# Kernel optimization log

Measured on AMD Instinct MI355X. Metric: run time of the kernel, lower is better.

The kernel has to match this reference:

```python
import jax, jax.numpy as jnp
import numpy as np
import math

S, B, E, H = 2048, 2, 1024, 16
D = E // H
LN_EPS = 1e-5


def setup_inputs() -> dict:
    key = jax.random.key(0)
    ks = jax.random.split(key, 8)
    src = jax.random.normal(ks[0], (S, B, E), dtype=jnp.float32)
    # causal attention mask: 1 = attend, 0 = masked
    src_mask = jnp.tril(jnp.ones((S, S), dtype=jnp.int32))
    in_proj_w = jax.random.normal(ks[1], (2 * E, E), dtype=jnp.float32) * 0.02
    in_proj_b = jnp.zeros((2 * E,), dtype=jnp.float32)
    out_proj_w = jax.random.normal(ks[2], (E, E), dtype=jnp.float32) * 0.02
    out_proj_b = jnp.zeros((E,), dtype=jnp.float32)
    ln_g = jnp.ones((E,), dtype=jnp.float32)
    ln_b = jnp.zeros((E,), dtype=jnp.float32)
    return {"src": src, "src_mask": src_mask, "in_proj_w": in_proj_w,
            "in_proj_b": in_proj_b, "out_proj_w": out_proj_w,
            "out_proj_b": out_proj_b, "ln_g": ln_g, "ln_b": ln_b}


def _layernorm(x, g, b):
    mu = jnp.mean(x, axis=-1, keepdims=True)
    var = jnp.mean(jnp.square(x - mu), axis=-1, keepdims=True)
    return (x - mu) * jax.lax.rsqrt(var + LN_EPS) * g + b


def reference(src, src_mask, in_proj_w, in_proj_b, out_proj_w, out_proj_b, ln_g, ln_b):
    # src: (S, B, E)
    x_norm = _layernorm(src, ln_g, ln_b)
    proj = jax.nn.silu(x_norm @ in_proj_w.T + in_proj_b)     # (S, B, 2E)
    qkv, u = jnp.split(proj, 2, axis=-1)                     # each (S, B, E)
    qkv = qkv.reshape(S, B, H, D)                            # q = k = v = qkv
    # scores: (B, H, S_q, S_k)
    scores = jnp.einsum('sbhd,tbhd->bhst', qkv, qkv) / math.sqrt(D)
    # torch does masked_fill(-inf) then silu; silu(-inf) -> 0 in the limit,
    # which is the intended semantics (masked positions contribute nothing).
    weights = jnp.where(src_mask[None, None, :, :] == 0, 0.0, jax.nn.silu(scores))
    # attn_dropout is identity at eval
    attn = jnp.einsum('bhst,tbhd->sbhd', weights, qkv).reshape(S, B, E)
    gated = attn * u
    out = src + (gated @ out_proj_w.T + out_proj_b)          # out_dropout = identity
    return out
```

## Files before the change

kernel.cpp:

```cpp
#include <hip/hip_runtime.h>


typedef __attribute__((ext_vector_type(8))) short  short8;
typedef __attribute__((ext_vector_type(4))) float  floatx4;
typedef __attribute__((ext_vector_type(4))) float  fvec4;
typedef __attribute__((ext_vector_type(4))) unsigned short usvec4;
typedef __attribute__((ext_vector_type(4))) int    intx4;

__device__ __forceinline__ unsigned short f2b(float f) {
  unsigned u = __builtin_bit_cast(unsigned, f);
  u += 0x7FFFu + ((u >> 16) & 1u);
  return (unsigned short)(u >> 16);
}
__device__ __forceinline__ float b2f(unsigned short h) {
  unsigned u = ((unsigned)h) << 16;
  return __builtin_bit_cast(float, u);
}
__device__ __forceinline__ float silu_f(float x) {
  float e = __builtin_amdgcn_exp2f(-1.44269504f * x);
  return x * __builtin_amdgcn_rcpf(1.f + e);
}
__device__ __forceinline__ void async_copy16(void* lds, const void* g) {
  __builtin_amdgcn_global_load_lds(
      (__attribute__((address_space(1))) void*)(g),
      (__attribute__((address_space(3))) void*)(lds), 16, 0, 0);
}

__global__ __launch_bounds__(256) void prep_kernel(
    const float* __restrict__ w1, unsigned short* __restrict__ w1b,
    const float* __restrict__ w2, unsigned short* __restrict__ w2b,
    const float* __restrict__ x, const float* __restrict__ g,
    const float* __restrict__ b, unsigned short* __restrict__ xn) {
  const int blk = blockIdx.x;
  if (blk < 3072) {
    int i = blk * 256 + threadIdx.x;
    const float* s; unsigned short* d; int j;
    if (i < 524288) { s = w1; d = w1b; j = i; } else { s = w2; d = w2b; j = i - 524288; }
    fvec4 v = ((const fvec4*)s)[j];
    usvec4 o = { f2b(v.x), f2b(v.y), f2b(v.z), f2b(v.w) };
    ((usvec4*)d)[j] = o;
    return;
  }
  const int lane = threadIdx.x & 63;
  const int row = (blk - 3072) * 4 + (threadIdx.x >> 6);
  const fvec4* xr = (const fvec4*)(x + (long)row * 1024);
  fvec4 v[4];
  float s = 0.f, s2 = 0.f;
  #pragma unroll
  for (int c = 0; c < 4; ++c) {
    v[c] = xr[lane + 64 * c];
    s  += v[c].x + v[c].y + v[c].z + v[c].w;
    s2 += v[c].x*v[c].x + v[c].y*v[c].y + v[c].z*v[c].z + v[c].w*v[c].w;
  }
  #pragma unroll
  for (int off = 32; off; off >>= 1) { s += __shfl_xor(s, off); s2 += __shfl_xor(s2, off); }
  float mu  = s * (1.f / 1024.f);
  float var = s2 * (1.f / 1024.f) - mu * mu;
  float rs  = rsqrtf(var + 1e-5f);
  usvec4* outr = (usvec4*)(xn + (long)row * 1024);
  #pragma unroll
  for (int c = 0; c < 4; ++c) {
    fvec4 gg = ((const fvec4*)g)[lane + 64 * c];
    fvec4 bb = ((const fvec4*)b)[lane + 64 * c];
    usvec4 o = { f2b((v[c].x - mu) * rs * gg.x + bb.x),
                 f2b((v[c].y - mu) * rs * gg.y + bb.y),
                 f2b((v[c].z - mu) * rs * gg.z + bb.z),
                 f2b((v[c].w - mu) * rs * gg.w + bb.w) };
    outr[lane + 64 * c] = o;
  }
}

__global__ __launch_bounds__(256, 2) void gemm_in(
    const unsigned short* __restrict__ A, const unsigned short* __restrict__ Bw,
    const float* __restrict__ bias,
    unsigned short* __restrict__ out0, unsigned short* __restrict__ out1) {
  __shared__ __align__(16) unsigned short sA[2][128 * 32];
  __shared__ __align__(16) unsigned short sB[2][128 * 32];
  const int t = threadIdx.x;
  const int lane = t & 63, l15 = lane & 15, quad = lane >> 4;
  const int w = t >> 6, wm = w >> 1, wn = w & 1;
  const int m0 = blockIdx.y * 128, n0 = blockIdx.x * 128;
  const int K = 1024;

  floatx4 acc[4][4];
  const floatx4 z4 = {0.f, 0.f, 0.f, 0.f};
  #pragma unroll
  for (int i = 0; i < 4; i++)
    #pragma unroll
    for (int j = 0; j < 4; j++) acc[i][j] = z4;

  for (int kt = 0; kt < 16; ++kt) {
    const int k0 = kt << 6;
    __syncthreads();
    #pragma unroll
    for (int h = 0; h < 2; ++h) {
      #pragma unroll
      for (int c = 0; c < 2; ++c) {
        int slot = c * 256 + t;
        int row = slot >> 2, col = (slot & 3) << 3;
        async_copy16(&sA[h][slot * 8], &A[(m0 + row) * K + k0 + h * 32 + col]);
        async_copy16(&sB[h][slot * 8], &Bw[(n0 + row) * K + k0 + h * 32 + col]);
      }
    }
    __syncthreads();
    #pragma unroll
    for (int h = 0; h < 2; ++h) {
      short8 af[4], bf[4];
      #pragma unroll
      for (int mr = 0; mr < 4; mr++)
        af[mr] = *(const short8*)&sA[h][(wm * 64 + mr * 16 + l15) * 32 + quad * 8];
      #pragma unroll
      for (int nr = 0; nr < 4; nr++)
        bf[nr] = *(const short8*)&sB[h][(wn * 64 + nr * 16 + l15) * 32 + quad * 8];
      #pragma unroll
      for (int mr = 0; mr < 4; mr++)
        #pragma unroll
        for (int nr = 0; nr < 4; nr++)
          acc[mr][nr] = __builtin_amdgcn_mfma_f32_16x16x32_bf16(af[mr], bf[nr], acc[mr][nr], 0, 0, 0);
    }
  }

  #pragma unroll
  for (int mr = 0; mr < 4; mr++) {
    int gm0 = m0 + wm * 64 + mr * 16 + quad * 4;
    #pragma unroll
    for (int nr = 0; nr < 4; nr++) {
      int gn = n0 + wn * 64 + nr * 16 + l15;
      float bv = bias[gn];
      unsigned short* dst = (gn < 1024) ? (out0 + gn) : (out1 + gn - 1024);
      #pragma unroll
      for (int r = 0; r < 4; r++) {
        float v = acc[mr][nr][r] + bv;
        dst[(long)(gm0 + r) * 1024] = f2b(silu_f(v));
      }
    }
  }
}

__global__ __launch_bounds__(256, 2) void gemm_out(
    const unsigned short* __restrict__ A, const unsigned short* __restrict__ Bw,
    const float* __restrict__ bias, const float* __restrict__ src,
    float* __restrict__ outf) {
  __shared__ __align__(16) unsigned short sA[2][128 * 32];
  __shared__ __align__(16) unsigned short sB[2][64 * 32];
  const int t = threadIdx.x;
  const int lane = t & 63, l15 = lane & 15, quad = lane >> 4;
  const int w = t >> 6;
  const int m0 = blockIdx.y * 128, n0 = blockIdx.x * 64;

  floatx4 acc[2][4];
  const floatx4 z4 = {0.f, 0.f, 0.f, 0.f};
  #pragma unroll
  for (int i = 0; i < 2; i++)
    #pragma unroll
    for (int j = 0; j < 4; j++) acc[i][j] = z4;

  for (int kt = 0; kt < 16; ++kt) {
    const int k0 = kt << 6;
    __syncthreads();
    #pragma unroll
    for (int h = 0; h < 2; ++h) {
      #pragma unroll
      for (int c = 0; c < 2; ++c) {
        int slot = c * 256 + t;
        int row = slot >> 2, col = (slot & 3) << 3;
        async_copy16(&sA[h][slot * 8], &A[(m0 + row) * 1024 + k0 + h * 32 + col]);
      }
      { int row = t >> 2, col = (t & 3) << 3;
        async_copy16(&sB[h][t * 8], &Bw[(n0 + row) * 1024 + k0 + h * 32 + col]); }
    }
    __syncthreads();
    #pragma unroll
    for (int h = 0; h < 2; ++h) {
      short8 af[2], bf[4];
      #pragma unroll
      for (int mr = 0; mr < 2; mr++)
        af[mr] = *(const short8*)&sA[h][(w * 32 + mr * 16 + l15) * 32 + quad * 8];
      #pragma unroll
      for (int nr = 0; nr < 4; nr++)
        bf[nr] = *(const short8*)&sB[h][(nr * 16 + l15) * 32 + quad * 8];
      #pragma unroll
      for (int mr = 0; mr < 2; mr++)
        #pragma unroll
        for (int nr = 0; nr < 4; nr++)
          acc[mr][nr] = __builtin_amdgcn_mfma_f32_16x16x32_bf16(af[mr], bf[nr], acc[mr][nr], 0, 0, 0);
    }
  }

  #pragma unroll
  for (int mr = 0; mr < 2; mr++) {
    int gm0 = m0 + w * 32 + mr * 16 + quad * 4;
    #pragma unroll
    for (int nr = 0; nr < 4; nr++) {
      int gn = n0 + nr * 16 + l15;
      float bv = bias[gn];
      #pragma unroll
      for (int r = 0; r < 4; r++) {
        long idx = (long)(gm0 + r) * 1024 + gn;
        outf[idx] = acc[mr][nr][r] + bv + src[idx];
      }
    }
  }
}

#define SKS 72
#define SVS 136
__device__ __forceinline__ void write_kv(unsigned short* sKp, unsigned short* sVp,
                                         const short8* kv, int rg, int dg, int swz0) {
  #pragma unroll
  for (int i = 0; i < 4; ++i)
    *(short8*)&sKp[(rg * 4 + i) * SKS + dg * 8] = kv[i];
  intx4 k0 = __builtin_bit_cast(intx4, kv[0]);
  intx4 k1 = __builtin_bit_cast(intx4, kv[1]);
  intx4 k2 = __builtin_bit_cast(intx4, kv[2]);
  intx4 k3 = __builtin_bit_cast(intx4, kv[3]);
  #pragma unroll
  for (int jj = 0; jj < 4; ++jj) {
    unsigned lo = __builtin_amdgcn_perm((unsigned)k1[jj], (unsigned)k0[jj], 0x05040100u);
    unsigned hi = __builtin_amdgcn_perm((unsigned)k3[jj], (unsigned)k2[jj], 0x05040100u);
    int j = 2 * jj, d = dg * 8 + j;
    int gsw = (swz0 + j) & 15;
    *(unsigned long long*)&sVp[d * SVS + gsw * 8 + (rg & 1) * 4] =
        (unsigned long long)lo | ((unsigned long long)hi << 32);
    lo = __builtin_amdgcn_perm((unsigned)k1[jj], (unsigned)k0[jj], 0x07060302u);
    hi = __builtin_amdgcn_perm((unsigned)k3[jj], (unsigned)k2[jj], 0x07060302u);
    j = 2 * jj + 1; d = dg * 8 + j;
    gsw = (swz0 + j) & 15;
    *(unsigned long long*)&sVp[d * SVS + gsw * 8 + (rg & 1) * 4] =
        (unsigned long long)lo | ((unsigned long long)hi << 32);
  }
}

__global__ __launch_bounds__(256, 2) void attn_kernel(
    const unsigned short* __restrict__ qkv, const unsigned short* __restrict__ u,
    unsigned short* __restrict__ gated) {
  __shared__ __align__(16) unsigned char smem[18432 + 2 * 17408];
  unsigned short* sK   = (unsigned short*)smem;
  unsigned short* sVt0 = (unsigned short*)(smem + 18432);
  unsigned short* sVt1 = (unsigned short*)(smem + 18432 + 17408);
  unsigned short* sQ   = sVt1;
  float*          sR   = (float*)smem;

  const int t = threadIdx.x, lane = t & 63, l15 = lane & 15, quad = lane >> 4;
  const int w = t >> 6;
  const int pair = blockIdx.x >> 5, bh = blockIdx.x & 31;
  const int b = bh >> 4, h = bh & 15;
  const long base = (long)b * 1024 + h * 64;
  const int rg = t >> 3, dg = t & 7;
  const int swz0 = (rg >> 1) + dg;
  const int addr_lo = 4 * (l15 + 32 * (quad & 1));
  const int addr_hi = addr_lo + 64;
  const bool qhi = quad >= 2;
  const int vswz = w * 4 + quad + (l15 & 7) + (l15 >> 3);
  const floatx4 z4 = {0.f, 0.f, 0.f, 0.f};

  for (int half = 0; half < 2; ++half) {
    const int qi = half ? (31 - pair) : pair;
    const int q0 = qi * 64;
    const int nkt = (qi >> 1) + 1;
    const bool evq = !(qi & 1);

    if (half) __syncthreads();
    #pragma unroll
    for (int c = 0; c < 2; ++c) {
      int slot = c * 256 + t, row = slot >> 3, cg = slot & 7;
      *(short8*)&sQ[row * SKS + cg * 8] =
          *(const short8*)&qkv[base + (long)(q0 + row) * 2048 + cg * 8];
    }
    __syncthreads();
    short8 qf[4][2];
    #pragma unroll
    for (int nt = 0; nt < 4; nt++)
      #pragma unroll
      for (int ks = 0; ks < 2; ks++)
        qf[nt][ks] = *(const short8*)&sQ[(nt * 16 + l15) * SKS + ks * 32 + quad * 8];
    short8 kv[4];
    #pragma unroll
    for (int i = 0; i < 4; ++i)
      kv[i] = *(const short8*)&qkv[base + (long)(rg * 4 + i) * 2048 + dg * 8];
    write_kv(sK, sVt0, kv, rg, dg, swz0);

    floatx4 oacc[4][4];
    #pragma unroll
    for (int i = 0; i < 4; i++)
      #pragma unroll
      for (int j = 0; j < 4; j++) oacc[i][j] = z4;

    for (int kt = 0; kt < nkt; ++kt) {
      unsigned short* sVtC = (kt & 1) ? sVt1 : sVt0;
      unsigned short* sVtN = (kt & 1) ? sVt0 : sVt1;
      __syncthreads();
      const bool more = (kt + 1 < nkt);
      const bool stage_half = evq && (kt + 2 == nkt);
      const bool do_stage = more && (!stage_half || rg < 16);
      if (do_stage) {
        const long nb = base + (long)((kt + 1) * 128) * 2048;
        #pragma unroll
        for (int i = 0; i < 4; ++i)
          kv[i] = *(const short8*)&qkv[nb + (long)(rg * 4 + i) * 2048 + dg * 8];
      }
      const bool diag = (kt == nkt - 1);
      const bool skipw = diag && evq && (w >= 2);
      short8 kf[2][2];
      if (!skipw) {
        #pragma unroll
        for (int mt = 0; mt < 2; mt++)
          #pragma unroll
          for (int ks = 0; ks < 2; ks++)
            kf[mt][ks] = *(const short8*)&sK[(w * 32 + mt * 16 + l15) * SKS + ks * 32 + quad * 8];
      }
      __syncthreads();
      if (!skipw) {
        floatx4 sacc[2][4];
        #pragma unroll
        for (int i = 0; i < 2; i++)
          #pragma unroll
          for (int j = 0; j < 4; j++) sacc[i][j] = z4;
        #pragma unroll
        for (int ks = 0; ks < 2; ++ks)
          #pragma unroll
          for (int mt = 0; mt < 2; mt++)
            #pragma unroll
            for (int nt = 0; nt < 4; nt++)
              sacc[mt][nt] = __builtin_amdgcn_mfma_f32_16x16x32_bf16(
                  kf[mt][ks], qf[nt][ks], sacc[mt][nt], 0, 0, 0);
        const int tw = kt * 128 + w * 32;
        unsigned p0[2][4], p1[2][4];
        #pragma unroll
        for (int mt = 0; mt < 2; mt++)
          #pragma unroll
          for (int nt = 0; nt < 4; nt++) {
            float v[4];
            if (diag) {
              int qq = q0 + nt * 16 + l15;
              #pragma unroll
              for (int r = 0; r < 4; r++) {
                int tt = tw + mt * 16 + quad * 4 + r;
                float x = silu_f(sacc[mt][nt][r] * 0.125f);
                v[r] = (qq < tt) ? 0.f : x;
              }
            } else {
              #pragma unroll
              for (int r = 0; r < 4; r++) v[r] = silu_f(sacc[mt][nt][r] * 0.125f);
            }
            p0[mt][nt] = __builtin_amdgcn_perm(__builtin_bit_cast(unsigned, v[1]),
                                               __builtin_bit_cast(unsigned, v[0]), 0x07060302u);
            p1[mt][nt] = __builtin_amdgcn_perm(__builtin_bit_cast(unsigned, v[3]),
                                               __builtin_bit_cast(unsigned, v[2]), 0x07060302u);
          }
        short8 vb[4];
        #pragma unroll
        for (int dt = 0; dt < 4; dt++)
          vb[dt] = *(const short8*)&sVtC[(dt * 16 + l15) * SVS + ((vswz + 2 * dt) & 15) * 8];
        #pragma unroll
        for (int qt = 0; qt < 4; qt++) {
          intx4 pa;
          #pragma unroll
          for (int jj = 0; jj < 4; jj++) {
            int addr = (jj >> 1) ? addr_hi : addr_lo;
            int lo, hi;
            if (jj & 1) {
              lo = __builtin_amdgcn_ds_bpermute(addr, (int)p1[0][qt]);
              hi = __builtin_amdgcn_ds_bpermute(addr, (int)p1[1][qt]);
            } else {
              lo = __builtin_amdgcn_ds_bpermute(addr, (int)p0[0][qt]);
              hi = __builtin_amdgcn_ds_bpermute(addr, (int)p0[1][qt]);
            }
            pa[jj] = qhi ? hi : lo;
          }
          short8 paf = __builtin_bit_cast(short8, pa);
          #pragma unroll
          for (int dt = 0; dt < 4; dt++)
            oacc[qt][dt] = __builtin_amdgcn_mfma_f32_16x16x32_bf16(paf, vb[dt], oacc[qt][dt], 0, 0, 0);
        }
      }
      if (do_stage) write_kv(sK, sVtN, kv, rg, dg, swz0);
    }

    __syncthreads();
    float* plane = sR + (w & 1) * 4352;
    if (w < 2) {
      #pragma unroll
      for (int qt = 0; qt < 4; qt++)
        #pragma unroll
        for (int dt = 0; dt < 4; dt++)
          #pragma unroll
          for (int r = 0; r < 4; r++)
            plane[(qt * 16 + quad * 4 + r) * 68 + dt * 16 + l15] = oacc[qt][dt][r];
    }
    __syncthreads();
    if (w >= 2) {
      #pragma unroll
      for (int qt = 0; qt < 4; qt++)
        #pragma unroll
        for (int dt = 0; dt < 4; dt++)
          #pragma unroll
          for (int r = 0; r < 4; r++)
            plane[(qt * 16 + quad * 4 + r) * 68 + dt * 16 + l15] += oacc[qt][dt][r];
    }
    __syncthreads();
    {
      const int erow = t >> 2, edg = t & 3;
      const long grow = (long)(q0 + erow) * 2048 + base + edg * 16;
      short8 u0 = *(const short8*)&u[grow];
      short8 u1 = *(const short8*)&u[grow + 8];
      const float* r0p = sR + erow * 68 + edg * 16;
      const float* r1p = r0p + 4352;
      float o[16];
      #pragma unroll
      for (int c = 0; c < 4; c++) {
        fvec4 a = ((const fvec4*)r0p)[c];
        fvec4 bsum = ((const fvec4*)r1p)[c];
        o[4*c+0] = a.x + bsum.x; o[4*c+1] = a.y + bsum.y;
        o[4*c+2] = a.z + bsum.z; o[4*c+3] = a.w + bsum.w;
      }
      short8 g0, g1;
      #pragma unroll
      for (int j = 0; j < 8; ++j) {
        g0[j] = (short)f2b(o[j]     * b2f((unsigned short)u0[j]));
        g1[j] = (short)f2b(o[j + 8] * b2f((unsigned short)u1[j]));
      }
      *(short8*)&gated[grow]     = g0;
      *(short8*)&gated[grow + 8] = g1;
    }
  }
}

extern "C" void kernel_launch(void* const* d_in, const int* in_sizes, int n_in,
                              void* d_out, int out_size, void* d_ws, size_t ws_size,
                              hipStream_t stream) {
  const float* src = (const float*)d_in[0];
  const float* w1  = (const float*)d_in[2];
  const float* b1  = (const float*)d_in[3];
  const float* w2  = (const float*)d_in[4];
  const float* b2  = (const float*)d_in[5];
  const float* lng = (const float*)d_in[6];
  const float* lnb = (const float*)d_in[7];
  float* out = (float*)d_out;

  char* ws = (char*)d_ws;
  unsigned short* xn    = (unsigned short*)(ws + 0);
  unsigned short* qkv   = (unsigned short*)(ws + 8388608);
  unsigned short* uu    = (unsigned short*)(ws + 16777216);
  unsigned short* gated = (unsigned short*)(ws + 25165824);
  unsigned short* w1b   = (unsigned short*)(ws + 33554432);
  unsigned short* w2b   = (unsigned short*)(ws + 37748736);

  prep_kernel<<<4096, 256, 0, stream>>>(w1, w1b, w2, w2b, src, lng, lnb, xn);
  gemm_in<<<dim3(16, 32), 256, 0, stream>>>(xn, w1b, b1, qkv, uu);
  attn_kernel<<<512, 256, 0, stream>>>(qkv, uu, gated);
  gemm_out<<<dim3(16, 32), 256, 0, stream>>>(gated, w2b, b2, src, out);
}
```

Measured before the change: 185.7 us.

## Drop LDS staging of K/V; have each wave read key tiles directly from global

Removes the shared-memory K and transposed-V double buffers, the Q staging, and the per-tile block barriers in the attention kernel. Each wave now strides over 32-row key tiles independently and loads Q, K and V fragments straight from global memory, with V gathered through scalar 2-byte loads. This gets rid of the synchronisation and LDS transpose work. In exchange each wave issues many uncoalesced narrow global loads, and no K/V data is shared across waves.

```diff
diff --git a/kernel.cpp b/kernel.cpp
--- a/kernel.cpp
+++ b/kernel.cpp
@@ -203,82 +203,34 @@
   }
 }
 
-#define SKS 72
-#define SVS 136
-__device__ __forceinline__ void write_kv(unsigned short* sKp, unsigned short* sVp,
-                                         const short8* kv, int rg, int dg, int swz0) {
-  #pragma unroll
-  for (int i = 0; i < 4; ++i)
-    *(short8*)&sKp[(rg * 4 + i) * SKS + dg * 8] = kv[i];
-  intx4 k0 = __builtin_bit_cast(intx4, kv[0]);
-  intx4 k1 = __builtin_bit_cast(intx4, kv[1]);
-  intx4 k2 = __builtin_bit_cast(intx4, kv[2]);
-  intx4 k3 = __builtin_bit_cast(intx4, kv[3]);
-  #pragma unroll
-  for (int jj = 0; jj < 4; ++jj) {
-    unsigned lo = __builtin_amdgcn_perm((unsigned)k1[jj], (unsigned)k0[jj], 0x05040100u);
-    unsigned hi = __builtin_amdgcn_perm((unsigned)k3[jj], (unsigned)k2[jj], 0x05040100u);
-    int j = 2 * jj, d = dg * 8 + j;
-    int gsw = (swz0 + j) & 15;
-    *(unsigned long long*)&sVp[d * SVS + gsw * 8 + (rg & 1) * 4] =
-        (unsigned long long)lo | ((unsigned long long)hi << 32);
-    lo = __builtin_amdgcn_perm((unsigned)k1[jj], (unsigned)k0[jj], 0x07060302u);
-    hi = __builtin_amdgcn_perm((unsigned)k3[jj], (unsigned)k2[jj], 0x07060302u);
-    j = 2 * jj + 1; d = dg * 8 + j;
-    gsw = (swz0 + j) & 15;
-    *(unsigned long long*)&sVp[d * SVS + gsw * 8 + (rg & 1) * 4] =
-        (unsigned long long)lo | ((unsigned long long)hi << 32);
-  }
-}
-
 __global__ __launch_bounds__(256, 2) void attn_kernel(
     const unsigned short* __restrict__ qkv, const unsigned short* __restrict__ u,
     unsigned short* __restrict__ gated) {
-  __shared__ __align__(16) unsigned char smem[18432 + 2 * 17408];
-  unsigned short* sK   = (unsigned short*)smem;
-  unsigned short* sVt0 = (unsigned short*)(smem + 18432);
-  unsigned short* sVt1 = (unsigned short*)(smem + 18432 + 17408);
-  unsigned short* sQ   = sVt1;
-  float*          sR   = (float*)smem;
+  __shared__ __align__(16) float sR[2 * 64 * 68];
 
   const int t = threadIdx.x, lane = t & 63, l15 = lane & 15, quad = lane >> 4;
   const int w = t >> 6;
   const int pair = blockIdx.x >> 5, bh = blockIdx.x & 31;
   const int b = bh >> 4, h = bh & 15;
   const long base = (long)b * 1024 + h * 64;
-  const int rg = t >> 3, dg = t & 7;
-  const int swz0 = (rg >> 1) + dg;
   const int addr_lo = 4 * (l15 + 32 * (quad & 1));
   const int addr_hi = addr_lo + 64;
   const bool qhi = quad >= 2;
-  const int vswz = w * 4 + quad + (l15 & 7) + (l15 >> 3);
   const floatx4 z4 = {0.f, 0.f, 0.f, 0.f};
 
   for (int half = 0; half < 2; ++half) {
     const int qi = half ? (31 - pair) : pair;
     const int q0 = qi * 64;
-    const int nkt = (qi >> 1) + 1;
-    const bool evq = !(qi & 1);
+    const int ntk = 2 * qi + 2;
 
     if (half) __syncthreads();
-    #pragma unroll
-    for (int c = 0; c < 2; ++c) {
-      int slot = c * 256 + t, row = slot >> 3, cg = slot & 7;
-      *(short8*)&sQ[row * SKS + cg * 8] =
-          *(const short8*)&qkv[base + (long)(q0 + row) * 2048 + cg * 8];
-    }
-    __syncthreads();
+
     short8 qf[4][2];
     #pragma unroll
     for (int nt = 0; nt < 4; nt++)
       #pragma unroll
       for (int ks = 0; ks < 2; ks++)
-        qf[nt][ks] = *(const short8*)&sQ[(nt * 16 + l15) * SKS + ks * 32 + quad * 8];
-    short8 kv[4];
-    #pragma unroll
-    for (int i = 0; i < 4; ++i)
-      kv[i] = *(const short8*)&qkv[base + (long)(rg * 4 + i) * 2048 + dg * 8];
-    write_kv(sK, sVt0, kv, rg, dg, swz0);
+        qf[nt][ks] = *(const short8*)&qkv[base + (long)(q0 + nt * 16 + l15) * 2048 + ks * 32 + quad * 8];
 
     floatx4 oacc[4][4];
     #pragma unroll
@@ -286,95 +238,79 @@
       #pragma unroll
       for (int j = 0; j < 4; j++) oacc[i][j] = z4;
 
-    for (int kt = 0; kt < nkt; ++kt) {
-      unsigned short* sVtC = (kt & 1) ? sVt1 : sVt0;
-      unsigned short* sVtN = (kt & 1) ? sVt0 : sVt1;
-      __syncthreads();
-      const bool more = (kt + 1 < nkt);
-      const bool stage_half = evq && (kt + 2 == nkt);
-      const bool do_stage = more && (!stage_half || rg < 16);
-      if (do_stage) {
-        const long nb = base + (long)((kt + 1) * 128) * 2048;
-        #pragma unroll
-        for (int i = 0; i < 4; ++i)
-          kv[i] = *(const short8*)&qkv[nb + (long)(rg * 4 + i) * 2048 + dg * 8];
-      }
-      const bool diag = (kt == nkt - 1);
-      const bool skipw = diag && evq && (w >= 2);
+    for (int j = w; j < ntk; j += 4) {
+      const int t0 = j * 32;
       short8 kf[2][2];
-      if (!skipw) {
+      #pragma unroll
+      for (int mt = 0; mt < 2; mt++)
+        #pragma unroll
+        for (int ks = 0; ks < 2; ks++)
+          kf[mt][ks] = *(const short8*)&qkv[base + (long)(t0 + mt * 16 + l15) * 2048 + ks * 32 + quad * 8];
+      short8 vb[4];
+      #pragma unroll
+      for (int dt = 0; dt < 4; dt++) {
+        #pragma unroll
+        for (int jj = 0; jj < 8; jj++)
+          vb[dt][jj] = (short)qkv[base + (long)(t0 + quad * 8 + jj) * 2048 + dt * 16 + l15];
+      }
+      floatx4 sacc[2][4];
+      #pragma unroll
+      for (int i = 0; i < 2; i++)
+        #pragma unroll
+        for (int jn = 0; jn < 4; jn++) sacc[i][jn] = z4;
+      #pragma unroll
+      for (int ks = 0; ks < 2; ++ks)
         #pragma unroll
         for (int mt = 0; mt < 2; mt++)
           #pragma unroll
-          for (int ks = 0; ks < 2; ks++)
-            kf[mt][ks] = *(const short8*)&sK[(w * 32 + mt * 16 + l15) * SKS + ks * 32 + quad * 8];
-      }
-      __syncthreads();
-      if (!skipw) {
-        floatx4 sacc[2][4];
-        #pragma unroll
-        for (int i = 0; i < 2; i++)
-          #pragma unroll
-          for (int j = 0; j < 4; j++) sacc[i][j] = z4;
-        #pragma unroll
-        for (int ks = 0; ks < 2; ++ks)
-          #pragma unroll
-          for (int mt = 0; mt < 2; mt++)
+          for (int nt = 0; nt < 4; nt++)
+            sacc[mt][nt] = __builtin_amdgcn_mfma_f32_16x16x32_bf16(
+                kf[mt][ks], qf[nt][ks], sacc[mt][nt], 0, 0, 0);
+      const bool diag = (t0 >= q0);
+      unsigned p0[2][4], p1[2][4];
+      #pragma unroll
+      for (int mt = 0; mt < 2; mt++)
+        #pragma unroll
+        for (int nt = 0; nt < 4; nt++) {
+          float v[4];
+          if (diag) {
+            int qq = q0 + nt * 16 + l15;
             #pragma unroll
-            for (int nt = 0; nt < 4; nt++)
-              sacc[mt][nt] = __builtin_amdgcn_mfma_f32_16x16x32_bf16(
-                  kf[mt][ks], qf[nt][ks], sacc[mt][nt], 0, 0, 0);
-        const int tw = kt * 128 + w * 32;
-        unsigned p0[2][4], p1[2][4];
-        #pragma unroll
-        for (int mt = 0; mt < 2; mt++)
-          #pragma unroll
-          for (int nt = 0; nt < 4; nt++) {
-            float v[4];
-            if (diag) {
-              int qq = q0 + nt * 16 + l15;
-              #pragma unroll
-              for (int r = 0; r < 4; r++) {
-                int tt = tw + mt * 16 + quad * 4 + r;
-                float x = silu_f(sacc[mt][nt][r] * 0.125f);
-                v[r] = (qq < tt) ? 0.f : x;
-              }
-            } else {
-              #pragma unroll
-              for (int r = 0; r < 4; r++) v[r] = silu_f(sacc[mt][nt][r] * 0.125f);
+            for (int r = 0; r < 4; r++) {
+              int tt = t0 + mt * 16 + quad * 4 + r;
+              float x = silu_f(sacc[mt][nt][r] * 0.125f);
+              v[r] = (qq < tt) ? 0.f : x;
             }
-            p0[mt][nt] = __builtin_amdgcn_perm(__builtin_bit_cast(unsigned, v[1]),
-                                               __builtin_bit_cast(unsigned, v[0]), 0x07060302u);
-            p1[mt][nt] = __builtin_amdgcn_perm(__builtin_bit_cast(unsigned, v[3]),
-                                               __builtin_bit_cast(unsigned, v[2]), 0x07060302u);
+          } else {
+            #pragma unroll
+            for (int r = 0; r < 4; r++) v[r] = silu_f(sacc[mt][nt][r] * 0.125f);
           }
-        short8 vb[4];
+          p0[mt][nt] = __builtin_amdgcn_perm(__builtin_bit_cast(unsigned, v[1]),
+                                             __builtin_bit_cast(unsigned, v[0]), 0x07060302u);
+          p1[mt][nt] = __builtin_amdgcn_perm(__builtin_bit_cast(unsigned, v[3]),
+                                             __builtin_bit_cast(unsigned, v[2]), 0x07060302u);
+        }
+      #pragma unroll
+      for (int qt = 0; qt < 4; qt++) {
+        intx4 pa;
+        #pragma unroll
+        for (int jj = 0; jj < 4; jj++) {
+          int addr = (jj >> 1) ? addr_hi : addr_lo;
+          int lo, hi;
+          if (jj & 1) {
+            lo = __builtin_amdgcn_ds_bpermute(addr, (int)p1[0][qt]);
+            hi = __builtin_amdgcn_ds_bpermute(addr, (int)p1[1][qt]);
+          } else {
+            lo = __builtin_amdgcn_ds_bpermute(addr, (int)p0[0][qt]);
+            hi = __builtin_amdgcn_ds_bpermute(addr, (int)p0[1][qt]);
+          }
+          pa[jj] = qhi ? hi : lo;
+        }
+        short8 paf = __builtin_bit_cast(short8, pa);
         #pragma unroll
         for (int dt = 0; dt < 4; dt++)
-          vb[dt] = *(const short8*)&sVtC[(dt * 16 + l15) * SVS + ((vswz + 2 * dt) & 15) * 8];
-        #pragma unroll
-        for (int qt = 0; qt < 4; qt++) {
-          intx4 pa;
-          #pragma unroll
-          for (int jj = 0; jj < 4; jj++) {
-            int addr = (jj >> 1) ? addr_hi : addr_lo;
-            int lo, hi;
-            if (jj & 1) {
-              lo = __builtin_amdgcn_ds_bpermute(addr, (int)p1[0][qt]);
-              hi = __builtin_amdgcn_ds_bpermute(addr, (int)p1[1][qt]);
-            } else {
-              lo = __builtin_amdgcn_ds_bpermute(addr, (int)p0[0][qt]);
-              hi = __builtin_amdgcn_ds_bpermute(addr, (int)p0[1][qt]);
-            }
-            pa[jj] = qhi ? hi : lo;
-          }
-          short8 paf = __builtin_bit_cast(short8, pa);
-          #pragma unroll
-          for (int dt = 0; dt < 4; dt++)
-            oacc[qt][dt] = __builtin_amdgcn_mfma_f32_16x16x32_bf16(paf, vb[dt], oacc[qt][dt], 0, 0, 0);
-        }
-      }
-      if (do_stage) write_kv(sK, sVtN, kv, rg, dg, swz0);
+          oacc[qt][dt] = __builtin_amdgcn_mfma_f32_16x16x32_bf16(paf, vb[dt], oacc[qt][dt], 0, 0, 0);
+      }
     }
 
     __syncthreads();
```

After: 187.0 us. No clear change (+0.7%).
